# Optimization experiments

Hardware: AMD Instinct MI355X
Metric: run time of the kernel (lower is better)

Reference implementation:

```python
import jax, jax.numpy as jnp
import numpy as np

N_E = 1024      # codes per sub-codebook
E_DIM = 64      # code dimension
BETA = 0.25     # commitment cost (VectorQuantizer(n_e, e_dim, 0.25))


def setup_inputs() -> dict:
    key = jax.random.key(0)
    k1, k2 = jax.random.split(key)
    bs, c, h, w = 16, 512, 32, 32
    m = c // E_DIM  # 8 sub-codebooks
    z = jax.random.normal(k1, (bs, c, h, w), dtype=jnp.float32)
    # taming-style init: uniform(-1/n_e, 1/n_e)
    codebooks = jax.random.uniform(
        k2, (m, N_E, E_DIM), dtype=jnp.float32,
        minval=-1.0 / N_E, maxval=1.0 / N_E)
    return {"z": z, "codebooks": codebooks}


def reference(z, codebooks):
    bs, c, h, w = z.shape
    m, n_e, e_dim = codebooks.shape
    N = bs * h * w
    # [bs,c,h,w] -> [bs,h,w,c] -> [m, N, e_dim]: batched over all m sub-codebooks at once
    zf = z.transpose(0, 2, 3, 1).reshape(N, m, e_dim).transpose(1, 0, 2)

    # squared L2 distances: ||z||^2 + ||e||^2 - 2 z.e   -> [m, N, n_e]
    d = ((zf ** 2).sum(-1, keepdims=True)
         + (codebooks ** 2).sum(-1)[:, None, :]
         - 2.0 * jnp.einsum('mnd,mkd->mnk', zf, codebooks))
    idx = jnp.argmin(d, axis=-1)  # [m, N]

    # gather nearest codes: [m, N, e_dim]
    zq = jnp.take_along_axis(codebooks, idx[:, :, None], axis=1)

    # per-sub-codebook VQ loss, summed over m (loss = sum(loss_list))
    codebook_loss = jnp.mean((jax.lax.stop_gradient(zq) - zf) ** 2, axis=(1, 2))
    commit_loss = jnp.mean((zq - jax.lax.stop_gradient(zf)) ** 2, axis=(1, 2))
    loss = jnp.sum(codebook_loss + BETA * commit_loss)

    # straight-through estimator
    zq_st = zf + jax.lax.stop_gradient(zq - zf)

    # reassemble: [m,N,d] -> [N,m*d] -> [bs,h,w,c] -> [bs,c,h,w]
    z_vq = zq_st.transpose(1, 0, 2).reshape(bs, h, w, c).transpose(0, 3, 1, 2)

    # concat of per-codebook index tensors along dim 0
    min_encoding_indices = idx.reshape(-1)  # [m*N]
    # per-code occupancy counts summed over the m codebooks -> [n_e]
    bin_count = jnp.zeros((n_e,), jnp.int32).at[min_encoding_indices].add(1)

    return z_vq, loss, min_encoding_indices, bin_count
```

## Files before the change

### kernel.cpp

```cpp
#include <hip/hip_runtime.h>
#include <cfloat>

#define BS 16
#define CC 512
#define HWD 1024
#define NN 16384
#define MM 8
#define NE 1024
#define ED 64

#define LOSS_OFF 8388608
#define IDX_OFF  8388609
#define BIN_OFF  8519681

#define TAU 4e-5f
#define UWIN 400u

#define WS_B     0
#define WS_IDX   32768
#define WS_CAND  720928
#define WS_BMAT  3866656

typedef __attribute__((ext_vector_type(8))) short bf16x8;
typedef __attribute__((ext_vector_type(16))) float f32x16;

__device__ __forceinline__ unsigned short f2bf(float f) {
    unsigned int u = __float_as_uint(f);
    unsigned int r = (u + 0x7fffu + ((u >> 16) & 1u)) >> 16;
    return (unsigned short)r;
}
__device__ __forceinline__ float bf2f(unsigned short h) {
    return __uint_as_float(((unsigned int)h) << 16);
}
__device__ __forceinline__ unsigned umin_(unsigned a, unsigned b) { return a < b ? a : b; }
__device__ __forceinline__ unsigned umax_(unsigned a, unsigned b) { return a > b ? a : b; }
__device__ __forceinline__ unsigned umin3(unsigned a, unsigned b, unsigned c) {
    return umin_(umin_(a, b), c);
}

__device__ __forceinline__ float mul_rn(float a, float b) {
#pragma clang fp contract(off)
    return a * b;
}
__device__ __forceinline__ float add_rn(float a, float b) {
#pragma clang fp contract(off)
    return a + b;
}
__device__ __forceinline__ float sub_rn(float a, float b) {
#pragma clang fp contract(off)
    return a - b;
}

__device__ __forceinline__ float np_sumsq64(const float* x) {
    float r[8];
#pragma unroll
    for (int j = 0; j < 8; ++j) r[j] = mul_rn(x[j], x[j]);
#pragma unroll
    for (int i = 8; i < 64; i += 8) {
#pragma unroll
        for (int j = 0; j < 8; ++j) r[j] = add_rn(r[j], mul_rn(x[i + j], x[i + j]));
    }
    return add_rn(add_rn(add_rn(r[0], r[1]), add_rn(r[2], r[3])),
                  add_rn(add_rn(r[4], r[5]), add_rn(r[6], r[7])));
}

__device__ __forceinline__ float np_dot64(const float* zsh, const float4* cr4) {
    float v0 = 0.f, v1 = 0.f, v2 = 0.f, v3 = 0.f;
#pragma unroll
    for (int t = 0; t < 4; ++t) {
        float4 e0 = cr4[t * 4 + 0];
        float4 e1 = cr4[t * 4 + 1];
        float4 e2 = cr4[t * 4 + 2];
        float4 e3 = cr4[t * 4 + 3];
        const int d0 = 16 * t;
        v0 = add_rn(mul_rn(zsh[d0 + 0], e0.x),
             add_rn(mul_rn(zsh[d0 + 4], e1.x),
             add_rn(mul_rn(zsh[d0 + 8], e2.x),
             add_rn(mul_rn(zsh[d0 + 12], e3.x), v0))));
        v1 = add_rn(mul_rn(zsh[d0 + 1], e0.y),
             add_rn(mul_rn(zsh[d0 + 5], e1.y),
             add_rn(mul_rn(zsh[d0 + 9], e2.y),
             add_rn(mul_rn(zsh[d0 + 13], e3.y), v1))));
        v2 = add_rn(mul_rn(zsh[d0 + 2], e0.z),
             add_rn(mul_rn(zsh[d0 + 6], e1.z),
             add_rn(mul_rn(zsh[d0 + 10], e2.z),
             add_rn(mul_rn(zsh[d0 + 14], e3.z), v2))));
        v3 = add_rn(mul_rn(zsh[d0 + 3], e0.w),
             add_rn(mul_rn(zsh[d0 + 7], e1.w),
             add_rn(mul_rn(zsh[d0 + 11], e2.w),
             add_rn(mul_rn(zsh[d0 + 15], e3.w), v3))));
    }
    return add_rn(add_rn(v0, v1), add_rn(v2, v3));
}

__global__ __launch_bounds__(256) void prep_kernel(const float* __restrict__ cb,
                                                   float* __restrict__ Bhat,
                                                   uint4* __restrict__ Bmat,
                                                   float* __restrict__ out) {
    const int tid = threadIdx.x;
    if (blockIdx.x < 32) {
        int i = blockIdx.x * 256 + tid;
        if (i == 0) out[LOSS_OFF] = 0.0f;
        if (i < NE) out[BIN_OFF + i] = 0.0f;
        const float4* r4 = (const float4*)(cb + (size_t)i * ED);
        float x[ED];
#pragma unroll
        for (int q = 0; q < 16; ++q) {
            float4 v = r4[q];
            x[q*4+0] = v.x; x[q*4+1] = v.y; x[q*4+2] = v.z; x[q*4+3] = v.w;
        }
        Bhat[i] = np_sumsq64(x);
        return;
    }
    int t = (blockIdx.x - 32) * 256 + tid;
    int lane = t & 63;
    int ct = (t >> 6) & 31;
    int rem = t >> 11;
    int c = rem % 9;
    int m = rem / 9;
    int h = lane >> 5;
    int k = ct * 32 + (lane & 31);

    unsigned short v[8];
#pragma unroll
    for (int j = 0; j < 8; ++j) v[j] = 0;

    if (c < 8) {
        int d0 = 16 * (c & 3) + 8 * h;
        const float* e = cb + ((size_t)m * NE + k) * ED + d0;
#pragma unroll
        for (int j = 0; j < 8; ++j) {
            float f = -2.0f * e[j];
            unsigned short hi = f2bf(f);
            v[j] = (c >= 4) ? f2bf(f - bf2f(hi)) : hi;
        }
    } else if (h == 0) {
        const float* e = cb + ((size_t)m * NE + k) * ED;
        float s = 0.f;
#pragma unroll
        for (int d = 0; d < ED; ++d) s += e[d] * e[d];
        v[0] = f2bf(s);
        v[1] = 0x3F80;
    }
    uint4 o;
    o.x = (unsigned)v[0] | ((unsigned)v[1] << 16);
    o.y = (unsigned)v[2] | ((unsigned)v[3] << 16);
    o.z = (unsigned)v[4] | ((unsigned)v[5] << 16);
    o.w = (unsigned)v[6] | ((unsigned)v[7] << 16);
    Bmat[t] = o;
}

__global__ __launch_bounds__(512, 4) void argmin_kernel(
        const float* __restrict__ z, const uint4* __restrict__ Bmat,
        int* __restrict__ idx_out, unsigned short* __restrict__ cand) {
    const int tid = threadIdx.x;
    const int m = blockIdx.y;
    const int row0 = blockIdx.x * 256;
    const int w = tid >> 6;
    const int l = tid & 63;
    const int h = l >> 5;
    const int r5 = l & 31;

    __shared__ uint4 ldsB[3][9 * 2 * 64];

    const int n_mine = row0 + w * 32 + r5;
    const int b = n_mine >> 10;
    const int hw = n_mine & (HWD - 1);
    const float* zbase = z + (((size_t)(b * CC + m * ED)) << 10) + hw;

    bf16x8 zh[4], zl[4];
#pragma unroll
    for (int i = 0; i < 4; ++i) {
        int o = 2 * i + h;
#pragma unroll
        for (int j = 0; j < 8; ++j) {
            float f = zbase[(size_t)(8 * o + j) << 10];
            unsigned short hb = f2bf(f);
            unsigned short lb = f2bf(f - bf2f(hb));
            zh[i][j] = (short)hb;
            zl[i][j] = (short)lb;
        }
    }
    bf16x8 ones12 = {0, 0, 0, 0, 0, 0, 0, 0};
    if (h == 0) { ones12[0] = (short)0x3F80; ones12[1] = (short)0x3F80; }

    unsigned rbm = 0xFFFFFFF0u, rsec = 0xFFFFFFFFu, rinfo = 0;
    int ccnt = 0;
    unsigned cq0 = 0, cq1 = 0, cq2 = 0;
    auto push = [&](unsigned id) {
        cq2 = (cq2 << 16) | (cq1 >> 16);
        cq1 = (cq1 << 16) | (cq0 >> 16);
        cq0 = (cq0 << 16) | (id & 0xFFFFu);
        ccnt++;
    };

    auto stage = [&](int g, int bufi) {
        for (int seg = w; seg < 18; seg += 8) {
            int c = seg >> 1, ct2 = seg & 1;
            const uint4* src = Bmat +
                ((size_t)((m * 9 + c) * 32 + (g * 2 + ct2)) << 6) + l;
            uint4* dst = &ldsB[bufi][(c * 2 + ct2) * 64];
            __builtin_amdgcn_global_load_lds(
                (const __attribute__((address_space(1))) unsigned int*)src,
                (__attribute__((address_space(3))) unsigned int*)dst, 16, 0, 0);
        }
    };

    auto process = [&](const f32x16& acc, unsigned tile) {
        unsigned u[16];
#pragma unroll
        for (int s = 0; s < 16; ++s)
            u[s] = (__float_as_uint(acc[s]) & 0xFFFFFFF0u) | (unsigned)s;
        unsigned b0 = umin_(u[0], u[1]),  s0 = umax_(u[0], u[1]);
        unsigned b1 = umin_(u[2], u[3]),  s1 = umax_(u[2], u[3]);
        unsigned b2 = umin_(u[4], u[5]),  s2 = umax_(u[4], u[5]);
        unsigned b3 = umin_(u[6], u[7]),  s3 = umax_(u[6], u[7]);
        unsigned b4 = umin_(u[8], u[9]),  s4 = umax_(u[8], u[9]);
        unsigned b5 = umin_(u[10], u[11]), s5 = umax_(u[10], u[11]);
        unsigned b6 = umin_(u[12], u[13]), s6 = umax_(u[12], u[13]);
        unsigned b7 = umin_(u[14], u[15]), s7 = umax_(u[14], u[15]);
        unsigned B0 = umin_(b0, b1), S0 = umin3(umax_(b0, b1), s0, s1);
        unsigned B1 = umin_(b2, b3), S1 = umin3(umax_(b2, b3), s2, s3);
        unsigned B2 = umin_(b4, b5), S2 = umin3(umax_(b4, b5), s4, s5);
        unsigned B3 = umin_(b6, b7), S3 = umin3(umax_(b6, b7), s6, s7);
        unsigned C0 = umin_(B0, B1), T0 = umin3(umax_(B0, B1), S0, S1);
        unsigned C1 = umin_(B2, B3), T1 = umin3(umax_(B2, B3), S2, S3);
        unsigned bt = umin_(C0, C1), st = umin3(umax_(C0, C1), T0, T1);

        unsigned oldrbm = rbm;
        bool take = bt < oldrbm;
        unsigned newrbm = take ? bt : oldrbm;
        unsigned limit = newrbm + UWIN;
        rsec = umin3(rsec, st, take ? oldrbm : bt);
        int sbt = (int)(bt & 15u);
        if (take) {
            if (bt + UWIN < oldrbm) ccnt = 0;
            push(tile * 32u + ((unsigned)sbt & 3u) +
                 8u * ((unsigned)sbt >> 2) + 4u * (unsigned)h);
            rinfo = (tile << 4) | (unsigned)sbt;
        }
        rbm = newrbm;
        unsigned gatev = take ? st : bt;
        if (gatev < limit) {
#pragma unroll
            for (int s = 0; s < 16; ++s) {
                if (u[s] < limit && !(take && s == sbt))
                    push(tile * 32u + ((unsigned)s & 3u) +
                         8u * ((unsigned)s >> 2) + 4u * (unsigned)h);
            }
        }
    };

    stage(0, 0);
    stage(1, 1);
    asm volatile("s_waitcnt vmcnt(2)" ::: "memory");
    __builtin_amdgcn_s_barrier();

    int bR = 0;
    for (int g = 0; g < 16; ++g) {
        int bW = bR + 2; if (bW >= 3) bW -= 3;
        if (g < 14) stage(g + 2, bW);
        const uint4* Bb = &ldsB[bR][0];

        f32x16 a0, a1;
#pragma unroll
        for (int s = 0; s < 16; ++s) { a0[s] = 0.0f; a1[s] = 0.0f; }
        bf16x8 sh0[4], sh1[4];
        __builtin_amdgcn_s_setprio(1);
#pragma unroll
        for (int c = 0; c < 4; ++c) {
            bf16x8 af0 = *(const bf16x8*)&Bb[(c * 2 + 0) * 64 + l];
            bf16x8 af1 = *(const bf16x8*)&Bb[(c * 2 + 1) * 64 + l];
            sh0[c] = af0; sh1[c] = af1;
            a0 = __builtin_amdgcn_mfma_f32_32x32x16_bf16(af0, zh[c], a0, 0, 0, 0);
            a1 = __builtin_amdgcn_mfma_f32_32x32x16_bf16(af1, zh[c], a1, 0, 0, 0);
        }
#pragma unroll
        for (int c = 4; c < 8; ++c) {
            bf16x8 af0 = *(const bf16x8*)&Bb[(c * 2 + 0) * 64 + l];
            bf16x8 af1 = *(const bf16x8*)&Bb[(c * 2 + 1) * 64 + l];
            a0 = __builtin_amdgcn_mfma_f32_32x32x16_bf16(af0, zh[c & 3], a0, 0, 0, 0);
            a1 = __builtin_amdgcn_mfma_f32_32x32x16_bf16(af1, zh[c & 3], a1, 0, 0, 0);
        }
#pragma unroll
        for (int c = 0; c < 4; ++c) {
            a0 = __builtin_amdgcn_mfma_f32_32x32x16_bf16(sh0[c], zl[c], a0, 0, 0, 0);
            a1 = __builtin_amdgcn_mfma_f32_32x32x16_bf16(sh1[c], zl[c], a1, 0, 0, 0);
        }
        {
            bf16x8 af0 = *(const bf16x8*)&Bb[(8 * 2 + 0) * 64 + l];
            bf16x8 af1 = *(const bf16x8*)&Bb[(8 * 2 + 1) * 64 + l];
            a0 = __builtin_amdgcn_mfma_f32_32x32x16_bf16(af0, ones12, a0, 0, 0, 0);
            a1 = __builtin_amdgcn_mfma_f32_32x32x16_bf16(af1, ones12, a1, 0, 0, 0);
        }
        __builtin_amdgcn_s_setprio(0);
        process(a0, (unsigned)(g * 2 + 0));
        process(a1, (unsigned)(g * 2 + 1));

        if (g < 14) {
            asm volatile("s_waitcnt vmcnt(2)" ::: "memory");
        } else if (g == 14) {
            asm volatile("s_waitcnt vmcnt(0)" ::: "memory");
        }
        if (g < 15) __builtin_amdgcn_s_barrier();
        bR = (bR == 2) ? 0 : bR + 1;
    }

    unsigned short* myslots = cand + ((size_t)(m * NN + n_mine) * 2 + h) * 6;
    if (ccnt) {
        unsigned* cp = (unsigned*)myslots;
        cp[0] = cq0; cp[1] = cq1; cp[2] = cq2;
    }

    int pcnt = __shfl_xor(ccnt, 32, 64);

    unsigned ss = rinfo & 15u, tile = rinfo >> 4;
    int k = (int)(tile * 32 + (ss & 3u) + 8u * (ss >> 2) + 4u * (unsigned)h);
    unsigned orbm = __shfl_xor(rbm, 32, 64);
    int ok = __shfl_xor(k, 32, 64);
    unsigned orsec = __shfl_xor(rsec, 32, 64);
    bool take = orbm < rbm;
    unsigned lose = take ? rbm : orbm;
    unsigned fb = take ? orbm : rbm;
    int fk = take ? ok : k;
    unsigned fs = umin3(rsec, orsec, lose);
    if (l < 32) {
        int mn = m * NN + n_mine;
        int pack = fk;
        float margin = __uint_as_float(fs & 0xFFFFFFF0u) -
                       __uint_as_float(fb & 0xFFFFFFF0u);
        if (margin < TAU) {
            int c0 = ccnt > 6 ? 7 : ccnt;
            int c1 = pcnt > 6 ? 7 : pcnt;
            pack |= (1 << 30) | (c0 << 16) | (c1 << 20);
        }
        idx_out[mn] = pack;
    }
}

__global__ __launch_bounds__(256) void output_kernel(
        const float* __restrict__ z, const float* __restrict__ cb,
        const float* __restrict__ Bhat, const unsigned short* __restrict__ cand,
        const int* __restrict__ idx_in, float* __restrict__ out) {
    const int tid = threadIdx.x;
    const int lane = tid & 63;
    const int wv = tid >> 6;
    const int n = blockIdx.x * 256 + tid;
    const int m = blockIdx.y;
    const int row0 = blockIdx.x * 256;

    __shared__ int hist[NE];
    __shared__ int ridx[256];
    __shared__ int pks[256];
    __shared__ short flist[256];
    __shared__ int fcnt;
    __shared__ float zsh[4][ED];

    if (tid == 0) fcnt = 0;
#pragma unroll
    for (int i = 0; i < 4; ++i) hist[tid + i * 256] = 0;
    const int pk = idx_in[m * NN + n];
    pks[tid] = pk;
    ridx[tid] = pk & 1023;
    __syncthreads();
    if (pk & (1 << 30)) {
        int q = atomicAdd(&fcnt, 1);
        flist[q] = (short)tid;
    }
    __syncthreads();

    const int fc = fcnt;
    for (int r = wv; r < fc; r += 4) {
        const int t = flist[r];
        const int rn = row0 + t;
        const int rb = rn >> 10;
        const int rhw = rn & (HWD - 1);
        const int mn = m * NN + rn;
        const int c0 = (pks[t] >> 16) & 15;
        const int c1 = (pks[t] >> 20) & 15;

        zsh[wv][lane] = z[(((size_t)(rb * CC + m * ED + lane)) << 10) + rhw];
        float A = np_sumsq64(&zsh[wv][0]);

        int kk;
        if (c0 == 7 || c1 == 7) {
            const float* cbm = cb + (size_t)m * NE * ED;
            const float* Bm = Bhat + m * NE;
            float best = FLT_MAX;
            int bidx = NE;
            for (int i = 0; i < 16; ++i) {
                const int k = i * 64 + lane;
                const float4* cr4 = (const float4*)(cbm + (size_t)k * ED);
                float C = np_dot64(&zsh[wv][0], cr4);
                float dk = sub_rn(add_rn(A, Bm[k]), mul_rn(2.0f, C));
                if (dk < best || (dk == best && k < bidx)) { best = dk; bidx = k; }
            }
#pragma unroll
            for (int off = 32; off >= 1; off >>= 1) {
                float ov = __shfl_down(best, off, 64);
                int oi = __shfl_down(bidx, off, 64);
                if (ov < best || (ov == best && oi < bidx)) { best = ov; bidx = oi; }
            }
            kk = bidx;
        } else {
            int kj = -1;
            if (lane < c0) kj = cand[(size_t)mn * 12 + lane];
            else if (lane >= 8 && lane < 8 + c1)
                kj = cand[(size_t)mn * 12 + 6 + (lane - 8)];

            float dref = FLT_MAX;
            if (kj >= 0) {
                const float4* cr4 = (const float4*)(cb + ((size_t)m * NE + kj) * ED);
                float C = np_dot64(&zsh[wv][0], cr4);
                dref = sub_rn(add_rn(A, Bhat[m * NE + kj]), mul_rn(2.0f, C));
            }
            int ki = (kj >= 0) ? kj : NE;
#pragma unroll
            for (int off = 32; off >= 1; off >>= 1) {
                float ov = __shfl_down(dref, off, 64);
                int oi = __shfl_down(ki, off, 64);
                if (ov < dref || (ov == dref && oi < ki)) { dref = ov; ki = oi; }
            }
            kk = ki;
        }
        if (lane == 0) ridx[t] = kk;
    }
    __syncthreads();

    const int idx_row = ridx[tid];
    out[IDX_OFF + m * NN + n] = (float)idx_row;
    atomicAdd(&hist[idx_row], 1);

    const int b = n >> 10;
    const int hw0 = row0 & (HWD - 1);
    const int q = lane;
    const int i0 = ridx[4 * q + 0];
    const int i1 = ridx[4 * q + 1];
    const int i2 = ridx[4 * q + 2];
    const int i3 = ridx[4 * q + 3];
    const float* cr0 = cb + ((size_t)m * NE + i0) * ED;
    const float* cr1 = cb + ((size_t)m * NE + i1) * ED;
    const float* cr2 = cb + ((size_t)m * NE + i2) * ED;
    const float* cr3 = cb + ((size_t)m * NE + i3) * ED;

    double acc = 0.0;
#pragma unroll
    for (int dd = 0; dd < 16; ++dd) {
        const int d = 16 * wv + dd;
        const size_t off = (((size_t)(b * CC + m * ED + d)) << 10) + hw0 + 4 * q;
        float4 zz = *(const float4*)(z + off);
        float4 vv;
        vv.x = cr0[d]; vv.y = cr1[d]; vv.z = cr2[d]; vv.w = cr3[d];
        *(float4*)(out + off) = vv;
        float dx = vv.x - zz.x, dy = vv.y - zz.y;
        float dz2 = vv.z - zz.z, dw = vv.w - zz.w;
        acc += (double)dx * dx + (double)dy * dy;
        acc += (double)dz2 * dz2 + (double)dw * dw;
    }

#pragma unroll
    for (int off = 32; off >= 1; off >>= 1)
        acc += __shfl_down(acc, off, 64);
    __shared__ double wsum[4];
    if ((tid & 63) == 0) wsum[tid >> 6] = acc;
    __syncthreads();
    if (tid == 0) {
        double t = wsum[0] + wsum[1] + wsum[2] + wsum[3];
        atomicAdd(out + LOSS_OFF, (float)(t * (1.25 / 1048576.0)));
    }
    __syncthreads();
#pragma unroll
    for (int i = 0; i < 4; ++i) {
        int v = hist[tid + i * 256];
        if (v) atomicAdd(out + BIN_OFF + tid + i * 256, (float)v);
    }
}

extern "C" void kernel_launch(void* const* d_in, const int* in_sizes, int n_in,
                              void* d_out, int out_size, void* d_ws, size_t ws_size,
                              hipStream_t stream) {
    const float* z = (const float*)d_in[0];
    const float* cb = (const float*)d_in[1];
    float* out = (float*)d_out;
    char* ws = (char*)d_ws;
    float* Bhat = (float*)(ws + WS_B);
    int* idxw = (int*)(ws + WS_IDX);
    unsigned short* cand = (unsigned short*)(ws + WS_CAND);
    uint4* Bmat = (uint4*)(ws + WS_BMAT);

    prep_kernel<<<dim3(608), dim3(256), 0, stream>>>(cb, Bhat, Bmat, out);
    argmin_kernel<<<dim3(NN / 256, MM), dim3(512), 0, stream>>>(
        z, Bmat, idxw, cand);
    output_kernel<<<dim3(NN / 256, MM), dim3(256), 0, stream>>>(
        z, cb, Bhat, cand, idxw, out);
}
```

Baseline: 160.9 us.

## Fuse prep, argmin and output kernels into one cooperative persistent kernel

Merges the three launches into a single cooperative kernel. A grid-wide sync separates the codebook preprocessing from the argmin/output phase, and blocks loop persistently over (sub-codebook, row-tile) units. The candidate list and indices stay in shared memory instead of making a round trip through a global workspace, and the refinement and output stages now run inside the argmin block. This removes launch gaps and global traffic for the intermediates, but adds grid-sync cost, unions LDS between phases, and may reduce occupancy or the overlap between stages.

```diff
diff --git a/kernel.cpp b/kernel.cpp
--- a/kernel.cpp
+++ b/kernel.cpp
@@ -1,5 +1,8 @@
 #include <hip/hip_runtime.h>
+#include <hip/hip_cooperative_groups.h>
 #include <cfloat>
+
+namespace cg = cooperative_groups;
 
 #define BS 16
 #define CC 512
@@ -17,9 +20,9 @@
 #define UWIN 400u
 
 #define WS_B     0
-#define WS_IDX   32768
-#define WS_CAND  720928
 #define WS_BMAT  3866656
+
+#define PREP_TOTAL (MM * NE + MM * 9 * 2048)
 
 typedef __attribute__((ext_vector_type(8))) short bf16x8;
 typedef __attribute__((ext_vector_type(16))) float f32x16;
@@ -93,386 +96,387 @@
     return add_rn(add_rn(v0, v1), add_rn(v2, v3));
 }
 
-__global__ __launch_bounds__(256) void prep_kernel(const float* __restrict__ cb,
-                                                   float* __restrict__ Bhat,
-                                                   uint4* __restrict__ Bmat,
-                                                   float* __restrict__ out) {
+__global__ __launch_bounds__(512, 4) void fused_kernel(
+        const float* __restrict__ z, const float* __restrict__ cb,
+        float* __restrict__ Bhat, uint4* __restrict__ Bmat,
+        float* __restrict__ out) {
     const int tid = threadIdx.x;
-    if (blockIdx.x < 32) {
-        int i = blockIdx.x * 256 + tid;
-        if (i == 0) out[LOSS_OFF] = 0.0f;
-        if (i < NE) out[BIN_OFF + i] = 0.0f;
-        const float4* r4 = (const float4*)(cb + (size_t)i * ED);
-        float x[ED];
-#pragma unroll
-        for (int q = 0; q < 16; ++q) {
-            float4 v = r4[q];
-            x[q*4+0] = v.x; x[q*4+1] = v.y; x[q*4+2] = v.z; x[q*4+3] = v.w;
-        }
-        Bhat[i] = np_sumsq64(x);
-        return;
+    const int bid = blockIdx.x;
+    const int nblk = gridDim.x;
+
+    union SMem {
+        uint4 ldsB[3][9 * 2 * 64];
+        struct {
+            int hist[NE];
+            int ridx[256];
+            int pks[256];
+            short flist[256];
+            int fcnt;
+            float zsh[8][ED];
+            double wsum[8];
+            unsigned short candl[256][12];
+        } o;
+    };
+    __shared__ SMem sm;
+
+    for (int gt = bid * 512 + tid; gt < PREP_TOTAL; gt += nblk * 512) {
+        if (gt < MM * NE) {
+            if (gt == 0) out[LOSS_OFF] = 0.0f;
+            if (gt < NE) out[BIN_OFF + gt] = 0.0f;
+            const float4* r4 = (const float4*)(cb + (size_t)gt * ED);
+            float x[ED];
+#pragma unroll
+            for (int q = 0; q < 16; ++q) {
+                float4 v = r4[q];
+                x[q*4+0] = v.x; x[q*4+1] = v.y; x[q*4+2] = v.z; x[q*4+3] = v.w;
+            }
+            Bhat[gt] = np_sumsq64(x);
+        } else {
+            int t = gt - MM * NE;
+            int lane = t & 63;
+            int ct = (t >> 6) & 31;
+            int rem = t >> 11;
+            int c = rem % 9;
+            int mm = rem / 9;
+            int hh = lane >> 5;
+            int k = ct * 32 + (lane & 31);
+
+            unsigned short v[8];
+#pragma unroll
+            for (int j = 0; j < 8; ++j) v[j] = 0;
+            if (c < 8) {
+                int d0 = 16 * (c & 3) + 8 * hh;
+                const float* e = cb + ((size_t)mm * NE + k) * ED + d0;
+#pragma unroll
+                for (int j = 0; j < 8; ++j) {
+                    float f = -2.0f * e[j];
+                    unsigned short hi = f2bf(f);
+                    v[j] = (c >= 4) ? f2bf(f - bf2f(hi)) : hi;
+                }
+            } else if (hh == 0) {
+                const float* e = cb + ((size_t)mm * NE + k) * ED;
+                float s = 0.f;
+#pragma unroll
+                for (int d = 0; d < ED; ++d) s += e[d] * e[d];
+                v[0] = f2bf(s);
+                v[1] = 0x3F80;
+            }
+            uint4 o4;
+            o4.x = (unsigned)v[0] | ((unsigned)v[1] << 16);
+            o4.y = (unsigned)v[2] | ((unsigned)v[3] << 16);
+            o4.z = (unsigned)v[4] | ((unsigned)v[5] << 16);
+            o4.w = (unsigned)v[6] | ((unsigned)v[7] << 16);
+            Bmat[t] = o4;
+        }
     }
-    int t = (blockIdx.x - 32) * 256 + tid;
-    int lane = t & 63;
-    int ct = (t >> 6) & 31;
-    int rem = t >> 11;
-    int c = rem % 9;
-    int m = rem / 9;
-    int h = lane >> 5;
-    int k = ct * 32 + (lane & 31);
-
-    unsigned short v[8];
-#pragma unroll
-    for (int j = 0; j < 8; ++j) v[j] = 0;
-
-    if (c < 8) {
-        int d0 = 16 * (c & 3) + 8 * h;
-        const float* e = cb + ((size_t)m * NE + k) * ED + d0;
-#pragma unroll
-        for (int j = 0; j < 8; ++j) {
-            float f = -2.0f * e[j];
-            unsigned short hi = f2bf(f);
-            v[j] = (c >= 4) ? f2bf(f - bf2f(hi)) : hi;
-        }
-    } else if (h == 0) {
-        const float* e = cb + ((size_t)m * NE + k) * ED;
-        float s = 0.f;
-#pragma unroll
-        for (int d = 0; d < ED; ++d) s += e[d] * e[d];
-        v[0] = f2bf(s);
-        v[1] = 0x3F80;
-    }
-    uint4 o;
-    o.x = (unsigned)v[0] | ((unsigned)v[1] << 16);
-    o.y = (unsigned)v[2] | ((unsigned)v[3] << 16);
-    o.z = (unsigned)v[4] | ((unsigned)v[5] << 16);
-    o.w = (unsigned)v[6] | ((unsigned)v[7] << 16);
-    Bmat[t] = o;
-}
-
-__global__ __launch_bounds__(512, 4) void argmin_kernel(
-        const float* __restrict__ z, const uint4* __restrict__ Bmat,
-        int* __restrict__ idx_out, unsigned short* __restrict__ cand) {
-    const int tid = threadIdx.x;
-    const int m = blockIdx.y;
-    const int row0 = blockIdx.x * 256;
+    __threadfence();
+    cg::this_grid().sync();
+
     const int w = tid >> 6;
     const int l = tid & 63;
     const int h = l >> 5;
     const int r5 = l & 31;
 
-    __shared__ uint4 ldsB[3][9 * 2 * 64];
-
-    const int n_mine = row0 + w * 32 + r5;
-    const int b = n_mine >> 10;
-    const int hw = n_mine & (HWD - 1);
-    const float* zbase = z + (((size_t)(b * CC + m * ED)) << 10) + hw;
-
-    bf16x8 zh[4], zl[4];
-#pragma unroll
-    for (int i = 0; i < 4; ++i) {
-        int o = 2 * i + h;
-#pragma unroll
-        for (int j = 0; j < 8; ++j) {
-            float f = zbase[(size_t)(8 * o + j) << 10];
-            unsigned short hb = f2bf(f);
-            unsigned short lb = f2bf(f - bf2f(hb));
-            zh[i][j] = (short)hb;
-            zl[i][j] = (short)lb;
-        }
-    }
-    bf16x8 ones12 = {0, 0, 0, 0, 0, 0, 0, 0};
-    if (h == 0) { ones12[0] = (short)0x3F80; ones12[1] = (short)0x3F80; }
-
-    unsigned rbm = 0xFFFFFFF0u, rsec = 0xFFFFFFFFu, rinfo = 0;
-    int ccnt = 0;
-    unsigned cq0 = 0, cq1 = 0, cq2 = 0;
-    auto push = [&](unsigned id) {
-        cq2 = (cq2 << 16) | (cq1 >> 16);
-        cq1 = (cq1 << 16) | (cq0 >> 16);
-        cq0 = (cq0 << 16) | (id & 0xFFFFu);
-        ccnt++;
-    };
-
-    auto stage = [&](int g, int bufi) {
-        for (int seg = w; seg < 18; seg += 8) {
-            int c = seg >> 1, ct2 = seg & 1;
-            const uint4* src = Bmat +
-                ((size_t)((m * 9 + c) * 32 + (g * 2 + ct2)) << 6) + l;
-            uint4* dst = &ldsB[bufi][(c * 2 + ct2) * 64];
-            __builtin_amdgcn_global_load_lds(
-                (const __attribute__((address_space(1))) unsigned int*)src,
-                (__attribute__((address_space(3))) unsigned int*)dst, 16, 0, 0);
-        }
-    };
-
-    auto process = [&](const f32x16& acc, unsigned tile) {
-        unsigned u[16];
-#pragma unroll
-        for (int s = 0; s < 16; ++s)
-            u[s] = (__float_as_uint(acc[s]) & 0xFFFFFFF0u) | (unsigned)s;
-        unsigned b0 = umin_(u[0], u[1]),  s0 = umax_(u[0], u[1]);
-        unsigned b1 = umin_(u[2], u[3]),  s1 = umax_(u[2], u[3]);
-        unsigned b2 = umin_(u[4], u[5]),  s2 = umax_(u[4], u[5]);
-        unsigned b3 = umin_(u[6], u[7]),  s3 = umax_(u[6], u[7]);
-        unsigned b4 = umin_(u[8], u[9]),  s4 = umax_(u[8], u[9]);
-        unsigned b5 = umin_(u[10], u[11]), s5 = umax_(u[10], u[11]);
-        unsigned b6 = umin_(u[12], u[13]), s6 = umax_(u[12], u[13]);
-        unsigned b7 = umin_(u[14], u[15]), s7 = umax_(u[14], u[15]);
-        unsigned B0 = umin_(b0, b1), S0 = umin3(umax_(b0, b1), s0, s1);
-        unsigned B1 = umin_(b2, b3), S1 = umin3(umax_(b2, b3), s2, s3);
-        unsigned B2 = umin_(b4, b5), S2 = umin3(umax_(b4, b5), s4, s5);
-        unsigned B3 = umin_(b6, b7), S3 = umin3(umax_(b6, b7), s6, s7);
-        unsigned C0 = umin_(B0, B1), T0 = umin3(umax_(B0, B1), S0, S1);
-        unsigned C1 = umin_(B2, B3), T1 = umin3(umax_(B2, B3), S2, S3);
-        unsigned bt = umin_(C0, C1), st = umin3(umax_(C0, C1), T0, T1);
-
-        unsigned oldrbm = rbm;
-        bool take = bt < oldrbm;
-        unsigned newrbm = take ? bt : oldrbm;
-        unsigned limit = newrbm + UWIN;
-        rsec = umin3(rsec, st, take ? oldrbm : bt);
-        int sbt = (int)(bt & 15u);
-        if (take) {
-            if (bt + UWIN < oldrbm) ccnt = 0;
-            push(tile * 32u + ((unsigned)sbt & 3u) +
-                 8u * ((unsigned)sbt >> 2) + 4u * (unsigned)h);
-            rinfo = (tile << 4) | (unsigned)sbt;
-        }
-        rbm = newrbm;
-        unsigned gatev = take ? st : bt;
-        if (gatev < limit) {
-#pragma unroll
-            for (int s = 0; s < 16; ++s) {
-                if (u[s] < limit && !(take && s == sbt))
-                    push(tile * 32u + ((unsigned)s & 3u) +
-                         8u * ((unsigned)s >> 2) + 4u * (unsigned)h);
-            }
-        }
-    };
-
-    stage(0, 0);
-    stage(1, 1);
-    asm volatile("s_waitcnt vmcnt(2)" ::: "memory");
-    __builtin_amdgcn_s_barrier();
-
-    int bR = 0;
-    for (int g = 0; g < 16; ++g) {
-        int bW = bR + 2; if (bW >= 3) bW -= 3;
-        if (g < 14) stage(g + 2, bW);
-        const uint4* Bb = &ldsB[bR][0];
-
-        f32x16 a0, a1;
-#pragma unroll
-        for (int s = 0; s < 16; ++s) { a0[s] = 0.0f; a1[s] = 0.0f; }
-        bf16x8 sh0[4], sh1[4];
-        __builtin_amdgcn_s_setprio(1);
-#pragma unroll
-        for (int c = 0; c < 4; ++c) {
-            bf16x8 af0 = *(const bf16x8*)&Bb[(c * 2 + 0) * 64 + l];
-            bf16x8 af1 = *(const bf16x8*)&Bb[(c * 2 + 1) * 64 + l];
-            sh0[c] = af0; sh1[c] = af1;
-            a0 = __builtin_amdgcn_mfma_f32_32x32x16_bf16(af0, zh[c], a0, 0, 0, 0);
-            a1 = __builtin_amdgcn_mfma_f32_32x32x16_bf16(af1, zh[c], a1, 0, 0, 0);
-        }
-#pragma unroll
-        for (int c = 4; c < 8; ++c) {
-            bf16x8 af0 = *(const bf16x8*)&Bb[(c * 2 + 0) * 64 + l];
-            bf16x8 af1 = *(const bf16x8*)&Bb[(c * 2 + 1) * 64 + l];
-            a0 = __builtin_amdgcn_mfma_f32_32x32x16_bf16(af0, zh[c & 3], a0, 0, 0, 0);
-            a1 = __builtin_amdgcn_mfma_f32_32x32x16_bf16(af1, zh[c & 3], a1, 0, 0, 0);
-        }
-#pragma unroll
-        for (int c = 0; c < 4; ++c) {
-            a0 = __builtin_amdgcn_mfma_f32_32x32x16_bf16(sh0[c], zl[c], a0, 0, 0, 0);
-            a1 = __builtin_amdgcn_mfma_f32_32x32x16_bf16(sh1[c], zl[c], a1, 0, 0, 0);
-        }
+    for (int u = bid; u < 512; u += nblk) {
+        __syncthreads();
+        const int m = u >> 6;
+        const int row0 = (u & 63) * 256;
+
+        const int n_mine = row0 + w * 32 + r5;
+        const int b = n_mine >> 10;
+        const int hw = n_mine & (HWD - 1);
+        const float* zbase = z + (((size_t)(b * CC + m * ED)) << 10) + hw;
+
+        bf16x8 zh[4], zl[4];
+#pragma unroll
+        for (int i = 0; i < 4; ++i) {
+            int o = 2 * i + h;
+#pragma unroll
+            for (int j = 0; j < 8; ++j) {
+                float f = zbase[(size_t)(8 * o + j) << 10];
+                unsigned short hb = f2bf(f);
+                unsigned short lb = f2bf(f - bf2f(hb));
+                zh[i][j] = (short)hb;
+                zl[i][j] = (short)lb;
+            }
+        }
+        bf16x8 ones12 = {0, 0, 0, 0, 0, 0, 0, 0};
+        if (h == 0) { ones12[0] = (short)0x3F80; ones12[1] = (short)0x3F80; }
+
+        unsigned rbm = 0xFFFFFFF0u, rsec = 0xFFFFFFFFu, rinfo = 0;
+        int ccnt = 0;
+        unsigned cq0 = 0, cq1 = 0, cq2 = 0;
+        auto push = [&](unsigned id) {
+            cq2 = (cq2 << 16) | (cq1 >> 16);
+            cq1 = (cq1 << 16) | (cq0 >> 16);
+            cq0 = (cq0 << 16) | (id & 0xFFFFu);
+            ccnt++;
+        };
+
+        auto stage = [&](int g, int bufi) {
+            for (int seg = w; seg < 18; seg += 8) {
+                int c = seg >> 1, ct2 = seg & 1;
+                const uint4* src = Bmat +
+                    ((size_t)((m * 9 + c) * 32 + (g * 2 + ct2)) << 6) + l;
+                uint4* dst = &sm.ldsB[bufi][(c * 2 + ct2) * 64];
+                __builtin_amdgcn_global_load_lds(
+                    (const __attribute__((address_space(1))) unsigned int*)src,
+                    (__attribute__((address_space(3))) unsigned int*)dst, 16, 0, 0);
+            }
+        };
+
+        auto process = [&](const f32x16& acc, unsigned tile) {
+            unsigned uu[16];
+#pragma unroll
+            for (int s = 0; s < 16; ++s)
+                uu[s] = (__float_as_uint(acc[s]) & 0xFFFFFFF0u) | (unsigned)s;
+            unsigned b0 = umin_(uu[0], uu[1]),  s0 = umax_(uu[0], uu[1]);
+            unsigned b1 = umin_(uu[2], uu[3]),  s1 = umax_(uu[2], uu[3]);
+            unsigned b2 = umin_(uu[4], uu[5]),  s2 = umax_(uu[4], uu[5]);
+            unsigned b3 = umin_(uu[6], uu[7]),  s3 = umax_(uu[6], uu[7]);
+            unsigned b4 = umin_(uu[8], uu[9]),  s4 = umax_(uu[8], uu[9]);
+            unsigned b5 = umin_(uu[10], uu[11]), s5 = umax_(uu[10], uu[11]);
+            unsigned b6 = umin_(uu[12], uu[13]), s6 = umax_(uu[12], uu[13]);
+            unsigned b7 = umin_(uu[14], uu[15]), s7 = umax_(uu[14], uu[15]);
+            unsigned B0 = umin_(b0, b1), S0 = umin3(umax_(b0, b1), s0, s1);
+            unsigned B1 = umin_(b2, b3), S1 = umin3(umax_(b2, b3), s2, s3);
+            unsigned B2 = umin_(b4, b5), S2 = umin3(umax_(b4, b5), s4, s5);
+            unsigned B3 = umin_(b6, b7), S3 = umin3(umax_(b6, b7), s6, s7);
+            unsigned C0 = umin_(B0, B1), T0 = umin3(umax_(B0, B1), S0, S1);
+            unsigned C1 = umin_(B2, B3), T1 = umin3(umax_(B2, B3), S2, S3);
+            unsigned bt = umin_(C0, C1), st = umin3(umax_(C0, C1), T0, T1);
+
+            unsigned oldrbm = rbm;
+            bool take = bt < oldrbm;
+            unsigned newrbm = take ? bt : oldrbm;
+            unsigned limit = newrbm + UWIN;
+            rsec = umin3(rsec, st, take ? oldrbm : bt);
+            int sbt = (int)(bt & 15u);
+            if (take) {
+                if (bt + UWIN < oldrbm) ccnt = 0;
+                push(tile * 32u + ((unsigned)sbt & 3u) +
+                     8u * ((unsigned)sbt >> 2) + 4u * (unsigned)h);
+                rinfo = (tile << 4) | (unsigned)sbt;
+            }
+            rbm = newrbm;
+            unsigned gatev = take ? st : bt;
+            if (gatev < limit) {
+#pragma unroll
+                for (int s = 0; s < 16; ++s) {
+                    if (uu[s] < limit && !(take && s == sbt))
+                        push(tile * 32u + ((unsigned)s & 3u) +
+                             8u * ((unsigned)s >> 2) + 4u * (unsigned)h);
+                }
+            }
+        };
+
+        stage(0, 0);
+        stage(1, 1);
+        asm volatile("s_waitcnt vmcnt(2)" ::: "memory");
+        __builtin_amdgcn_s_barrier();
+
+        int bR = 0;
+        for (int g = 0; g < 16; ++g) {
+            int bW = bR + 2; if (bW >= 3) bW -= 3;
+            if (g < 14) stage(g + 2, bW);
+            const uint4* Bb = &sm.ldsB[bR][0];
+
+            f32x16 a0, a1;
+#pragma unroll
+            for (int s = 0; s < 16; ++s) { a0[s] = 0.0f; a1[s] = 0.0f; }
+            bf16x8 sh0[4], sh1[4];
+            __builtin_amdgcn_s_setprio(1);
+#pragma unroll
+            for (int c = 0; c < 4; ++c) {
+                bf16x8 af0 = *(const bf16x8*)&Bb[(c * 2 + 0) * 64 + l];
+                bf16x8 af1 = *(const bf16x8*)&Bb[(c * 2 + 1) * 64 + l];
+                sh0[c] = af0; sh1[c] = af1;
+                a0 = __builtin_amdgcn_mfma_f32_32x32x16_bf16(af0, zh[c], a0, 0, 0, 0);
+                a1 = __builtin_amdgcn_mfma_f32_32x32x16_bf16(af1, zh[c], a1, 0, 0, 0);
+            }
+#pragma unroll
+            for (int c = 4; c < 8; ++c) {
+                bf16x8 af0 = *(const bf16x8*)&Bb[(c * 2 + 0) * 64 + l];
+                bf16x8 af1 = *(const bf16x8*)&Bb[(c * 2 + 1) * 64 + l];
+                a0 = __builtin_amdgcn_mfma_f32_32x32x16_bf16(af0, zh[c & 3], a0, 0, 0, 0);
+                a1 = __builtin_amdgcn_mfma_f32_32x32x16_bf16(af1, zh[c & 3], a1, 0, 0, 0);
+            }
+#pragma unroll
+            for (int c = 0; c < 4; ++c) {
+                a0 = __builtin_amdgcn_mfma_f32_32x32x16_bf16(sh0[c], zl[c], a0, 0, 0, 0);
+                a1 = __builtin_amdgcn_mfma_f32_32x32x16_bf16(sh1[c], zl[c], a1, 0, 0, 0);
+            }
+            {
+                bf16x8 af0 = *(const bf16x8*)&Bb[(8 * 2 + 0) * 64 + l];
+                bf16x8 af1 = *(const bf16x8*)&Bb[(8 * 2 + 1) * 64 + l];
+                a0 = __builtin_amdgcn_mfma_f32_32x32x16_bf16(af0, ones12, a0, 0, 0, 0);
+                a1 = __builtin_amdgcn_mfma_f32_32x32x16_bf16(af1, ones12, a1, 0, 0, 0);
+            }
+            __builtin_amdgcn_s_setprio(0);
+            process(a0, (unsigned)(g * 2 + 0));
+            process(a1, (unsigned)(g * 2 + 1));
+
+            if (g < 14) {
+                asm volatile("s_waitcnt vmcnt(2)" ::: "memory");
+            } else if (g == 14) {
+                asm volatile("s_waitcnt vmcnt(0)" ::: "memory");
+            }
+            if (g < 15) __builtin_amdgcn_s_barrier();
+            bR = (bR == 2) ? 0 : bR + 1;
+        }
+
+        __syncthreads();
+
+        sm.o.hist[tid] = 0;
+        sm.o.hist[tid + 512] = 0;
+        if (tid == 0) sm.o.fcnt = 0;
+        const int lrow = w * 32 + r5;
+        if (ccnt) {
+            unsigned* cp = (unsigned*)&sm.o.candl[lrow][h * 6];
+            cp[0] = cq0; cp[1] = cq1; cp[2] = cq2;
+        }
+        int pcnt = __shfl_xor(ccnt, 32, 64);
         {
-            bf16x8 af0 = *(const bf16x8*)&Bb[(8 * 2 + 0) * 64 + l];
-            bf16x8 af1 = *(const bf16x8*)&Bb[(8 * 2 + 1) * 64 + l];
-            a0 = __builtin_amdgcn_mfma_f32_32x32x16_bf16(af0, ones12, a0, 0, 0, 0);
-            a1 = __builtin_amdgcn_mfma_f32_32x32x16_bf16(af1, ones12, a1, 0, 0, 0);
-        }
-        __builtin_amdgcn_s_setprio(0);
-        process(a0, (unsigned)(g * 2 + 0));
-        process(a1, (unsigned)(g * 2 + 1));
-
-        if (g < 14) {
-            asm volatile("s_waitcnt vmcnt(2)" ::: "memory");
-        } else if (g == 14) {
-            asm volatile("s_waitcnt vmcnt(0)" ::: "memory");
-        }
-        if (g < 15) __builtin_amdgcn_s_barrier();
-        bR = (bR == 2) ? 0 : bR + 1;
-    }
-
-    unsigned short* myslots = cand + ((size_t)(m * NN + n_mine) * 2 + h) * 6;
-    if (ccnt) {
-        unsigned* cp = (unsigned*)myslots;
-        cp[0] = cq0; cp[1] = cq1; cp[2] = cq2;
-    }
-
-    int pcnt = __shfl_xor(ccnt, 32, 64);
-
-    unsigned ss = rinfo & 15u, tile = rinfo >> 4;
-    int k = (int)(tile * 32 + (ss & 3u) + 8u * (ss >> 2) + 4u * (unsigned)h);
-    unsigned orbm = __shfl_xor(rbm, 32, 64);
-    int ok = __shfl_xor(k, 32, 64);
-    unsigned orsec = __shfl_xor(rsec, 32, 64);
-    bool take = orbm < rbm;
-    unsigned lose = take ? rbm : orbm;
-    unsigned fb = take ? orbm : rbm;
-    int fk = take ? ok : k;
-    unsigned fs = umin3(rsec, orsec, lose);
-    if (l < 32) {
-        int mn = m * NN + n_mine;
-        int pack = fk;
-        float margin = __uint_as_float(fs & 0xFFFFFFF0u) -
-                       __uint_as_float(fb & 0xFFFFFFF0u);
-        if (margin < TAU) {
-            int c0 = ccnt > 6 ? 7 : ccnt;
-            int c1 = pcnt > 6 ? 7 : pcnt;
-            pack |= (1 << 30) | (c0 << 16) | (c1 << 20);
-        }
-        idx_out[mn] = pack;
-    }
-}
-
-__global__ __launch_bounds__(256) void output_kernel(
-        const float* __restrict__ z, const float* __restrict__ cb,
-        const float* __restrict__ Bhat, const unsigned short* __restrict__ cand,
-        const int* __restrict__ idx_in, float* __restrict__ out) {
-    const int tid = threadIdx.x;
-    const int lane = tid & 63;
-    const int wv = tid >> 6;
-    const int n = blockIdx.x * 256 + tid;
-    const int m = blockIdx.y;
-    const int row0 = blockIdx.x * 256;
-
-    __shared__ int hist[NE];
-    __shared__ int ridx[256];
-    __shared__ int pks[256];
-    __shared__ short flist[256];
-    __shared__ int fcnt;
-    __shared__ float zsh[4][ED];
-
-    if (tid == 0) fcnt = 0;
-#pragma unroll
-    for (int i = 0; i < 4; ++i) hist[tid + i * 256] = 0;
-    const int pk = idx_in[m * NN + n];
-    pks[tid] = pk;
-    ridx[tid] = pk & 1023;
-    __syncthreads();
-    if (pk & (1 << 30)) {
-        int q = atomicAdd(&fcnt, 1);
-        flist[q] = (short)tid;
-    }
-    __syncthreads();
-
-    const int fc = fcnt;
-    for (int r = wv; r < fc; r += 4) {
-        const int t = flist[r];
-        const int rn = row0 + t;
-        const int rb = rn >> 10;
-        const int rhw = rn & (HWD - 1);
-        const int mn = m * NN + rn;
-        const int c0 = (pks[t] >> 16) & 15;
-        const int c1 = (pks[t] >> 20) & 15;
-
-        zsh[wv][lane] = z[(((size_t)(rb * CC + m * ED + lane)) << 10) + rhw];
-        float A = np_sumsq64(&zsh[wv][0]);
-
-        int kk;
-        if (c0 == 7 || c1 == 7) {
-            const float* cbm = cb + (size_t)m * NE * ED;
-            const float* Bm = Bhat + m * NE;
-            float best = FLT_MAX;
-            int bidx = NE;
-            for (int i = 0; i < 16; ++i) {
-                const int k = i * 64 + lane;
-                const float4* cr4 = (const float4*)(cbm + (size_t)k * ED);
-                float C = np_dot64(&zsh[wv][0], cr4);
-                float dk = sub_rn(add_rn(A, Bm[k]), mul_rn(2.0f, C));
-                if (dk < best || (dk == best && k < bidx)) { best = dk; bidx = k; }
-            }
-#pragma unroll
-            for (int off = 32; off >= 1; off >>= 1) {
-                float ov = __shfl_down(best, off, 64);
-                int oi = __shfl_down(bidx, off, 64);
-                if (ov < best || (ov == best && oi < bidx)) { best = ov; bidx = oi; }
-            }
-            kk = bidx;
-        } else {
-            int kj = -1;
-            if (lane < c0) kj = cand[(size_t)mn * 12 + lane];
-            else if (lane >= 8 && lane < 8 + c1)
-                kj = cand[(size_t)mn * 12 + 6 + (lane - 8)];
-
-            float dref = FLT_MAX;
-            if (kj >= 0) {
-                const float4* cr4 = (const float4*)(cb + ((size_t)m * NE + kj) * ED);
-                float C = np_dot64(&zsh[wv][0], cr4);
-                dref = sub_rn(add_rn(A, Bhat[m * NE + kj]), mul_rn(2.0f, C));
-            }
-            int ki = (kj >= 0) ? kj : NE;
-#pragma unroll
-            for (int off = 32; off >= 1; off >>= 1) {
-                float ov = __shfl_down(dref, off, 64);
-                int oi = __shfl_down(ki, off, 64);
-                if (ov < dref || (ov == dref && oi < ki)) { dref = ov; ki = oi; }
-            }
-            kk = ki;
-        }
-        if (lane == 0) ridx[t] = kk;
-    }
-    __syncthreads();
-
-    const int idx_row = ridx[tid];
-    out[IDX_OFF + m * NN + n] = (float)idx_row;
-    atomicAdd(&hist[idx_row], 1);
-
-    const int b = n >> 10;
-    const int hw0 = row0 & (HWD - 1);
-    const int q = lane;
-    const int i0 = ridx[4 * q + 0];
-    const int i1 = ridx[4 * q + 1];
-    const int i2 = ridx[4 * q + 2];
-    const int i3 = ridx[4 * q + 3];
-    const float* cr0 = cb + ((size_t)m * NE + i0) * ED;
-    const float* cr1 = cb + ((size_t)m * NE + i1) * ED;
-    const float* cr2 = cb + ((size_t)m * NE + i2) * ED;
-    const float* cr3 = cb + ((size_t)m * NE + i3) * ED;
-
-    double acc = 0.0;
-#pragma unroll
-    for (int dd = 0; dd < 16; ++dd) {
-        const int d = 16 * wv + dd;
-        const size_t off = (((size_t)(b * CC + m * ED + d)) << 10) + hw0 + 4 * q;
-        float4 zz = *(const float4*)(z + off);
-        float4 vv;
-        vv.x = cr0[d]; vv.y = cr1[d]; vv.z = cr2[d]; vv.w = cr3[d];
-        *(float4*)(out + off) = vv;
-        float dx = vv.x - zz.x, dy = vv.y - zz.y;
-        float dz2 = vv.z - zz.z, dw = vv.w - zz.w;
-        acc += (double)dx * dx + (double)dy * dy;
-        acc += (double)dz2 * dz2 + (double)dw * dw;
-    }
-
-#pragma unroll
-    for (int off = 32; off >= 1; off >>= 1)
-        acc += __shfl_down(acc, off, 64);
-    __shared__ double wsum[4];
-    if ((tid & 63) == 0) wsum[tid >> 6] = acc;
-    __syncthreads();
-    if (tid == 0) {
-        double t = wsum[0] + wsum[1] + wsum[2] + wsum[3];
-        atomicAdd(out + LOSS_OFF, (float)(t * (1.25 / 1048576.0)));
-    }
-    __syncthreads();
-#pragma unroll
-    for (int i = 0; i < 4; ++i) {
-        int v = hist[tid + i * 256];
-        if (v) atomicAdd(out + BIN_OFF + tid + i * 256, (float)v);
+            unsigned ss = rinfo & 15u, tile = rinfo >> 4;
+            int k = (int)(tile * 32 + (ss & 3u) + 8u * (ss >> 2) + 4u * (unsigned)h);
+            unsigned orbm = __shfl_xor(rbm, 32, 64);
+            int ok = __shfl_xor(k, 32, 64);
+            unsigned orsec = __shfl_xor(rsec, 32, 64);
+            bool take = orbm < rbm;
+            unsigned lose = take ? rbm : orbm;
+            unsigned fb = take ? orbm : rbm;
+            int fk = take ? ok : k;
+            unsigned fs = umin3(rsec, orsec, lose);
+            if (l < 32) {
+                int pack = fk;
+                float margin = __uint_as_float(fs & 0xFFFFFFF0u) -
+                               __uint_as_float(fb & 0xFFFFFFF0u);
+                if (margin < TAU) {
+                    int c0 = ccnt > 6 ? 7 : ccnt;
+                    int c1 = pcnt > 6 ? 7 : pcnt;
+                    pack |= (1 << 30) | (c0 << 16) | (c1 << 20);
+                }
+                sm.o.pks[lrow] = pack;
+            }
+        }
+        __syncthreads();
+
+        if (tid < 256) {
+            int pk = sm.o.pks[tid];
+            sm.o.ridx[tid] = pk & 1023;
+            if (pk & (1 << 30)) {
+                int q = atomicAdd(&sm.o.fcnt, 1);
+                sm.o.flist[q] = (short)tid;
+            }
+        }
+        __syncthreads();
+
+        const int fc = sm.o.fcnt;
+        for (int r = w; r < fc; r += 8) {
+            const int t = sm.o.flist[r];
+            const int rn = row0 + t;
+            const int rb = rn >> 10;
+            const int rhw = rn & (HWD - 1);
+            const int c0 = (sm.o.pks[t] >> 16) & 15;
+            const int c1 = (sm.o.pks[t] >> 20) & 15;
+
+            sm.o.zsh[w][l] = z[(((size_t)(rb * CC + m * ED + l)) << 10) + rhw];
+            float A = np_sumsq64(&sm.o.zsh[w][0]);
+
+            int kk;
+            if (c0 == 7 || c1 == 7) {
+                const float* cbm = cb + (size_t)m * NE * ED;
+                const float* Bm = Bhat + m * NE;
+                float best = FLT_MAX;
+                int bidx = NE;
+                for (int i = 0; i < 16; ++i) {
+                    const int k = i * 64 + l;
+                    const float4* cr4 = (const float4*)(cbm + (size_t)k * ED);
+                    float C = np_dot64(&sm.o.zsh[w][0], cr4);
+                    float dk = sub_rn(add_rn(A, Bm[k]), mul_rn(2.0f, C));
+                    if (dk < best || (dk == best && k < bidx)) { best = dk; bidx = k; }
+                }
+#pragma unroll
+                for (int off = 32; off >= 1; off >>= 1) {
+                    float ov = __shfl_down(best, off, 64);
+                    int oi = __shfl_down(bidx, off, 64);
+                    if (ov < best || (ov == best && oi < bidx)) { best = ov; bidx = oi; }
+                }
+                kk = bidx;
+            } else {
+                int kj = -1;
+                if (l < c0) kj = sm.o.candl[t][l];
+                else if (l >= 8 && l < 8 + c1) kj = sm.o.candl[t][6 + (l - 8)];
+
+                float dref = FLT_MAX;
+                if (kj >= 0) {
+                    const float4* cr4 = (const float4*)(cb + ((size_t)m * NE + kj) * ED);
+                    float C = np_dot64(&sm.o.zsh[w][0], cr4);
+                    dref = sub_rn(add_rn(A, Bhat[m * NE + kj]), mul_rn(2.0f, C));
+                }
+                int ki = (kj >= 0) ? kj : NE;
+#pragma unroll
+                for (int off = 32; off >= 1; off >>= 1) {
+                    float ov = __shfl_down(dref, off, 64);
+                    int oi = __shfl_down(ki, off, 64);
+                    if (ov < dref || (ov == dref && oi < ki)) { dref = ov; ki = oi; }
+                }
+                kk = ki;
+            }
+            if (l == 0) sm.o.ridx[t] = kk;
+        }
+        __syncthreads();
+
+        if (tid < 256) {
+            int ir = sm.o.ridx[tid];
+            out[IDX_OFF + m * NN + row0 + tid] = (float)ir;
+            atomicAdd(&sm.o.hist[ir], 1);
+        }
+
+        const int b2 = row0 >> 10;
+        const int hw0 = row0 & (HWD - 1);
+        const int q = l;
+        const int i0 = sm.o.ridx[4 * q + 0];
+        const int i1 = sm.o.ridx[4 * q + 1];
+        const int i2 = sm.o.ridx[4 * q + 2];
+        const int i3 = sm.o.ridx[4 * q + 3];
+        const float* cr0 = cb + ((size_t)m * NE + i0) * ED;
+        const float* cr1 = cb + ((size_t)m * NE + i1) * ED;
+        const float* cr2 = cb + ((size_t)m * NE + i2) * ED;
+        const float* cr3 = cb + ((size_t)m * NE + i3) * ED;
+
+        double acc = 0.0;
+#pragma unroll
+        for (int dd = 0; dd < 8; ++dd) {
+            const int d = 8 * w + dd;
+            const size_t off = (((size_t)(b2 * CC + m * ED + d)) << 10) + hw0 + 4 * q;
+            float4 zz = *(const float4*)(z + off);
+            float4 vv;
+            vv.x = cr0[d]; vv.y = cr1[d]; vv.z = cr2[d]; vv.w = cr3[d];
+            *(float4*)(out + off) = vv;
+            float dx = vv.x - zz.x, dy = vv.y - zz.y;
+            float dz2 = vv.z - zz.z, dw = vv.w - zz.w;
+            acc += (double)dx * dx + (double)dy * dy;
+            acc += (double)dz2 * dz2 + (double)dw * dw;
+        }
+#pragma unroll
+        for (int off = 32; off >= 1; off >>= 1)
+            acc += __shfl_down(acc, off, 64);
+        if (l == 0) sm.o.wsum[w] = acc;
+        __syncthreads();
+        if (tid == 0) {
+            double t2 = 0.0;
+#pragma unroll
+            for (int i = 0; i < 8; ++i) t2 += sm.o.wsum[i];
+            atomicAdd(out + LOSS_OFF, (float)(t2 * (1.25 / 1048576.0)));
+        }
+        __syncthreads();
+        {
+            int v0 = sm.o.hist[tid];
+            if (v0) atomicAdd(out + BIN_OFF + tid, (float)v0);
+            int v1 = sm.o.hist[tid + 512];
+            if (v1) atomicAdd(out + BIN_OFF + tid + 512, (float)v1);
+        }
     }
 }
 
@@ -484,13 +488,19 @@
     float* out = (float*)d_out;
     char* ws = (char*)d_ws;
     float* Bhat = (float*)(ws + WS_B);
-    int* idxw = (int*)(ws + WS_IDX);
-    unsigned short* cand = (unsigned short*)(ws + WS_CAND);
     uint4* Bmat = (uint4*)(ws + WS_BMAT);
 
-    prep_kernel<<<dim3(608), dim3(256), 0, stream>>>(cb, Bhat, Bmat, out);
-    argmin_kernel<<<dim3(NN / 256, MM), dim3(512), 0, stream>>>(
-        z, Bmat, idxw, cand);
-    output_kernel<<<dim3(NN / 256, MM), dim3(256), 0, stream>>>(
-        z, cb, Bhat, cand, idxw, out);
-}
+    static int g_grid = 0;
+    if (g_grid == 0) {
+        int nb = 0;
+        hipOccupancyMaxActiveBlocksPerMultiprocessor(&nb, fused_kernel, 512, 0);
+        if (nb < 1) nb = 1;
+        long cap = (long)nb * 256;
+        g_grid = cap < 512 ? (int)cap : 512;
+    }
+
+    void* args[] = { (void*)&z, (void*)&cb, (void*)&Bhat, (void*)&Bmat,
+                     (void*)&out };
+    hipLaunchCooperativeKernel((const void*)fused_kernel, dim3(g_grid),
+                               dim3(512), args, 0, stream);
+}
```

New measurement: 295.1 us. 1.83x slower.
